# Optimization experiments

Hardware: AMD Instinct MI355X
Metric: run time of the kernel (lower is better)

## Reference

```python
import jax, jax.numpy as jnp
import numpy as np

B, C, H, W = 16, 1, 512, 512
D, F, KH, KW = 4, 24, 5, 5   # numWienerFilters, output_features, reg-filter size
BKH, BKW = 9, 9              # blur kernel size
LB, UB = 1e-4, 1e-2


def psf2otf(psf, shape):
    # zero-pad psf to `shape`, circularly shift its center to (0,0), FFT
    kh, kw = psf.shape[-2], psf.shape[-1]
    pad = [(0, 0)] * (psf.ndim - 2) + [(0, shape[0] - kh), (0, shape[1] - kw)]
    p = jnp.pad(psf, pad)
    p = jnp.roll(p, shift=(-((kh - 1) // 2), -((kw - 1) // 2)), axis=(-2, -1))
    return jnp.fft.fft2(p)


def _taper_profile(proj, n):
    # autocorrelation of the psf projection, periodized to length n (MATLAB edgetaper)
    z = jnp.zeros(n - 1, proj.dtype).at[: proj.shape[0]].set(proj)
    zf = jnp.fft.fft(z)
    acf = jnp.real(jnp.fft.ifft(zf * jnp.conj(zf)))
    acf = jnp.concatenate([acf, acf[:1]])
    return acf / acf.max()


def _normalize_weights(w, scale):
    # WeightNormalization5D: zero-mean + L2-normalize over (C,kh,kw), times scale
    w = w - w.mean(axis=(2, 3, 4), keepdims=True)
    nrm = jnp.sqrt(jnp.sum(w * w, axis=(2, 3, 4), keepdims=True))
    return w * (scale[..., None, None, None] / nrm)


def setup_inputs():
    key = jax.random.key(0)
    ks = jax.random.split(key, 4)
    x = jax.random.uniform(ks[0], (B, C, H, W), jnp.float32)
    bk = jax.random.uniform(ks[1], (BKH, BKW), jnp.float32) + 1e-3
    bk = bk / bk.sum()  # normalized blur PSF
    stdn = jax.random.uniform(ks[2], (B,), jnp.float32) * 0.1 + 0.01
    conv_weights = jax.random.normal(ks[3], (D, F, C, KH, KW), jnp.float32)
    scale = jnp.full((D, F), 0.1, jnp.float32)
    alpha = jnp.log(jnp.logspace(np.log10(LB), np.log10(UB), D))[:, None].astype(jnp.float32)
    return {"x": x, "blur_kernel": bk, "stdn": stdn,
            "conv_weights": conv_weights, "scale": scale, "alpha": alpha}


def reference(x, blur_kernel, stdn, conv_weights, scale, alpha):
    kh, kw = blur_kernel.shape
    # getPad2RetainShape
    pt, pb = (kh + 1) // 2 - 1, kh - (kh + 1) // 2
    pl, pr = (kw + 1) // 2 - 1, kw - (kw + 1) // 2
    xp = jnp.pad(x, ((0, 0), (0, 0), (pt, pb), (pl, pr)), mode="symmetric")
    Hp, Wp = xp.shape[-2], xp.shape[-1]
    otf = psf2otf(blur_kernel, (Hp, Wp))                     # (Hp,Wp) complex
    # EdgeTaper: blend image with its circular blur near borders
    br = _taper_profile(blur_kernel.sum(axis=1), Hp)
    bc = _taper_profile(blur_kernel.sum(axis=0), Wp)
    taper = (1.0 - br)[:, None] * (1.0 - bc)[None, :]
    blurred = jnp.real(jnp.fft.ifft2(jnp.fft.fft2(xp) * otf))
    xp = taper * xp + (1.0 - taper) * blurred
    # regularization-filter OTFs
    w = _normalize_weights(conv_weights, scale)              # (D,F,C,kh,kw)
    G = psf2otf(w, (Hp, Wp))                                 # (D,F,C,Hp,Wp)
    S = jnp.sum(G.real ** 2 + G.imag ** 2, axis=1)           # (D,C,Hp,Wp)
    a = jnp.exp(alpha)[:, :, None, None]                     # (D,1,1,1)
    B2 = otf.real ** 2 + otf.imag ** 2                       # (Hp,Wp)
    denom = B2[None, None] + a * S                           # (D,C,Hp,Wp)
    Y = jnp.conj(otf) * jnp.fft.fft2(xp)                     # (B,C,Hp,Wp)
    Xf = Y[:, None] / denom[None]                            # (B,D,C,Hp,Wp)
    out = jnp.real(jnp.fft.ifft2(Xf))[..., pt:Hp - pb, pl:Wp - pr]
    # colored-noise std factor per (wiener filter, channel)
    cvar = jnp.mean(B2[None, None] / denom ** 2, axis=(-2, -1))   # (D,C)
    cvar = jnp.broadcast_to(cvar[None], (x.shape[0],) + cvar.shape)  # (B,D,C)
    cstdn = jnp.sqrt(stdn[:, None] ** 2 * cvar.mean(axis=2))        # (B,D)
    return out, cstdn
```

## Files before the change

kernel.cpp:

```cpp
#include <hip/hip_runtime.h>
#include <math.h>

#define NP    520
#define NN    (520*520)
#define HH    512
#define NPIX  (512*512)
#define NB    16
#define NPAIR 8
#define ND    4
#define NF    24
#define KS    544
#define RS    576
#define PLANE ((size_t)RS*KS)
#define S8P   (8*PLANE)
#define E9SZ  (NP*9)
#define CSZ   (ND*9*NP)
#define NBORD 18396
#define PADCH 5536
#define NBLK2 1057
#define TWO_PI 6.283185307179586f

typedef unsigned short u16;
typedef __attribute__((ext_vector_type(8))) short bf16x8;
typedef __attribute__((ext_vector_type(4))) float f32x4;

__device__ __forceinline__ int wrap520(int t){ t %= NP; return t < 0 ? t + NP : t; }

__device__ __forceinline__ u16 f2bf(float f){
  unsigned u = __float_as_uint(f);
  u += 0x7FFFu + ((u >> 16) & 1u);
  return (u16)(u >> 16);
}
__device__ __forceinline__ float bf2f(u16 h){
  return __uint_as_float(((unsigned)h) << 16);
}
__device__ __forceinline__ void gll16(const u16* g, u16* l){
  __builtin_amdgcn_global_load_lds(
      (const __attribute__((address_space(1))) void*)g,
      (__attribute__((address_space(3))) void*)l, 16, 0, 0);
}
template<int N> __device__ __forceinline__ void vmwait(){
  if constexpr (N == 0)       asm volatile("s_waitcnt vmcnt(0)" ::: "memory");
  else if constexpr (N == 4)  asm volatile("s_waitcnt vmcnt(4)" ::: "memory");
  else if constexpr (N == 6)  asm volatile("s_waitcnt vmcnt(6)" ::: "memory");
  else if constexpr (N == 8)  asm volatile("s_waitcnt vmcnt(8)" ::: "memory");
  else if constexpr (N == 12) asm volatile("s_waitcnt vmcnt(12)" ::: "memory");
}
#define MF(a,b,c) __builtin_amdgcn_mfma_f32_16x16x32_bf16((a),(b),(c),0,0,0)


__global__ __launch_bounds__(256) void zwb_k(u16* __restrict__ slabs,
                                             u16* __restrict__ wf, u16* __restrict__ wi){
  int idx = blockIdx.x*256 + threadIdx.x;
  const int nA = 16*PADCH;
  if (idx < nA){
    int pl = idx / PADCH, cc = idx % PADCH;
    int row, col;
    if (cc < 1728){ row = cc/3; col = 520 + (cc%3)*8; }
    else { int c2 = cc - 1728; row = 520 + c2/68; col = (c2%68)*8; }
    bf16x8 z = {0,0,0,0,0,0,0,0};
    *(bf16x8*)(slabs + (size_t)pl*PLANE + (size_t)row*KS + col) = z;
    return;
  }
  idx -= nA;
  if (idx >= (int)PLANE) return;
  int r = idx / KS, k = idx % KS;
  float fr=0.f, fi=0.f, ir=0.f, ii=0.f;
  if (r < NP && k < NP){
    int m = (int)(((long long)r * (long long)k) % NP);
    float ang = TWO_PI * (float)m / (float)NP;
    float s, c; sincosf(ang, &s, &c);
    fr = c; fi = -s;
    ir = c * (1.0f/NP); ii = s * (1.0f/NP);
  }
  wf[0*PLANE+idx] = f2bf(fr); wf[1*PLANE+idx] = f2bf(fi);
  wi[0*PLANE+idx] = f2bf(ir); wi[1*PLANE+idx] = f2bf(ii);
}

__global__ __launch_bounds__(256) void setup1_k(const float* __restrict__ bk,
                                                const float* __restrict__ cw,
                                                const float* __restrict__ scale,
                                                float* __restrict__ e9,
                                                float* __restrict__ r_row, float* __restrict__ r_col,
                                                float* __restrict__ wn){
  int idx = blockIdx.x*256 + threadIdx.x;
  if (idx < NP*9){
    int u = idx / 9, t = idx % 9;
    int m = wrap520(u*(t-4));
    float ang = TWO_PI * (float)m / (float)NP;
    float s, c; sincosf(ang, &s, &c);
    e9[idx] = c; e9[E9SZ + idx] = -s;
    return;
  }
  idx -= NP*9;
  if (idx < 18){
    int k = idx % 9;
    bool rowp = (idx < 9);
    float proj[9];
    for (int m = 0; m < 9; ++m){
      float a = 0.f;
      for (int j = 0; j < 9; ++j) a += rowp ? bk[m*9+j] : bk[j*9+m];
      proj[m] = a;
    }
    float acc = 0.f;
    for (int m = 0; m + k < 9; ++m) acc += proj[m] * proj[m+k];
    (rowp ? r_row : r_col)[k] = acc;
    return;
  }
  idx -= 18;
  if (idx >= ND*NF) return;
  const float* wp = cw + idx*25;
  float mean = 0.f;
  for (int k = 0; k < 25; ++k) mean += wp[k];
  mean *= (1.0f/25.0f);
  float ss = 0.f;
  for (int k = 0; k < 25; ++k){ float d = wp[k]-mean; ss += d*d; }
  float sc = scale[idx] / sqrtf(ss);
  for (int k = 0; k < 25; ++k) wn[idx*25+k] = (wp[k]-mean)*sc;
}

__global__ __launch_bounds__(256) void setup2_k(const float* __restrict__ bk,
                                                const float* __restrict__ e9,
                                                const float* __restrict__ wn,
                                                float* __restrict__ T, float* __restrict__ R){
  int idx = blockIdx.x*256 + threadIdx.x;
  if (idx < 9*NP){
    int i = idx / NP, v = idx % NP;
    float tr = 0.f, ti = 0.f;
    #pragma unroll
    for (int j = 0; j < 9; ++j){
      float w = bk[i*9+j];
      tr += w * e9[v*9+j];
      ti += w * e9[E9SZ + v*9+j];
    }
    T[idx] = tr; T[9*NP + idx] = ti;
    return;
  }
  idx -= 9*NP;
  if (idx >= ND*81) return;
  int d = idx / 81, t = idx % 81;
  int di = t/9 - 4, dj = t%9 - 4;
  int i0 = di > 0 ? di : 0, i1 = di < 0 ? 4+di : 4;
  int j0 = dj > 0 ? dj : 0, j1 = dj < 0 ? 4+dj : 4;
  float acc = 0.f;
  for (int f = 0; f < NF; ++f){
    const float* w = wn + (d*NF+f)*25;
    for (int i = i0; i <= i1; ++i)
      for (int j = j0; j <= j1; ++j)
        acc += w[i*5+j] * w[(i-di)*5 + (j-dj)];
  }
  R[idx] = acc;
}

__global__ void C_k(const float* __restrict__ R, const float* __restrict__ e9,
                    float* __restrict__ Ctab){
  int idx = blockIdx.x*blockDim.x + threadIdx.x;
  if (idx >= ND*9*NP) return;
  int v = idx % NP, t9 = idx / NP;
  int d = t9 / 9, t = t9 % 9;
  float cr = 0.f, ci = 0.f;
  #pragma unroll
  for (int s = 0; s < 9; ++s){
    float r = R[d*81 + t*9 + s];
    cr += r * e9[v*9+s];
    ci += r * e9[E9SZ + v*9+s];
  }
  Ctab[idx] = cr; Ctab[CSZ + idx] = ci;
}

__global__ __launch_bounds__(256) void denomMT2_k(
    const float* __restrict__ Tb, const float* __restrict__ e9,
    const float* __restrict__ Ctab, const float* __restrict__ alpha,
    float* __restrict__ MTre, float* __restrict__ MTim, float* __restrict__ pcv){
  __shared__ float e9r[2304], e9i[2304];
  __shared__ float red[256];
  const int tid = threadIdx.x;
  const int p = blockIdx.x*256 + tid;
  {
    int u0 = (blockIdx.x*256) % NP;
    for (int i = tid; i < 2304; i += 256){
      int row = i / 9, col = i % 9;
      int uu = u0 + row; if (uu >= NP) uu -= NP;
      e9r[i] = e9[uu*9 + col];
      e9i[i] = e9[E9SZ + uu*9 + col];
    }
  }
  __syncthreads();
  float contrib[ND] = {0.f, 0.f, 0.f, 0.f};
  if (p < NN){
    int v = p / NP;
    float er9[9], ei9[9];
    #pragma unroll
    for (int i = 0; i < 9; ++i){ er9[i] = e9r[tid*9+i]; ei9[i] = e9i[tid*9+i]; }
    float ar = 0.f, ai = 0.f;
    #pragma unroll
    for (int i = 0; i < 9; ++i){
      float tr = Tb[i*NP+v], ti = Tb[9*NP + i*NP+v];
      ar += er9[i]*tr - ei9[i]*ti;
      ai += er9[i]*ti + ei9[i]*tr;
    }
    float B2 = ar*ar + ai*ai;
    #pragma unroll
    for (int d = 0; d < ND; ++d){
      float S = 0.f;
      #pragma unroll
      for (int t = 0; t < 9; ++t)
        S += er9[t]*Ctab[(d*9+t)*NP + v] - ei9[t]*Ctab[CSZ + (d*9+t)*NP + v];
      float dv = B2 + expf(alpha[d]) * S;
      MTre[(size_t)d*NN + p] = ar / dv;
      MTim[(size_t)d*NN + p] = -ai / dv;
      contrib[d] = B2 / (dv*dv);
    }
  }
  for (int d = 0; d < ND; ++d){
    red[tid] = contrib[d]; __syncthreads();
    for (int s = 128; s > 0; s >>= 1){
      if (tid < s) red[tid] += red[tid+s];
      __syncthreads();
    }
    if (tid == 0) pcv[(size_t)blockIdx.x*ND + d] = red[0];
    __syncthreads();
  }
}

__global__ __launch_bounds__(256) void cstdn2_k(const float* __restrict__ stdn,
                                                const float* __restrict__ pcv,
                                                float* __restrict__ out){
  __shared__ float red[256];
  int t = threadIdx.x;
  int d = t & 3, ch = t >> 2;
  float acc = 0.f;
  for (int b = ch; b < NBLK2; b += 64) acc += pcv[(size_t)b*ND + d];
  red[t] = acc; __syncthreads();
  for (int s = 128; s >= 4; s >>= 1){
    if (t < s) red[t] += red[t+s];
    __syncthreads();
  }
  if (t < NB*ND){
    int b = t >> 2, d2 = t & 3;
    float s = stdn[b];
    out[(size_t)NB*ND*NPIX + t] = sqrtf(s*s*red[d2]*(1.0f/(float)NN));
  }
}

__global__ __launch_bounds__(256) void pad_tr_k(const float* __restrict__ x,
                                                u16* __restrict__ MA){
  __shared__ float tile[64][65];
  const int q  = blockIdx.z;
  const int r0 = blockIdx.y * 64;
  const int c0 = blockIdx.x * 64;
  const int t  = threadIdx.x;
  const float* xq = x + (size_t)q*NPIX;
  const int jl = t & 63, ib = t >> 6;
  const bool fast = (c0 >= 64 && c0 <= 448 && r0 >= 64 && r0 <= 448);

  if (fast){
    #pragma unroll 1
    for (int pass = 0; pass < 16; ++pass){
      int il = ib + pass*4;
      tile[il][jl] = xq[(size_t)(c0+il-4)*HH + (r0+jl-4)];
    }
  } else {
    #pragma unroll 1
    for (int pass = 0; pass < 16; ++pass){
      int il = ib + pass*4;
      int I = c0 + il, J = r0 + jl;
      float v = 0.f;
      if (I < NP && J < NP){
        int si = I - 4; si = (si < 0) ? (-si-1) : ((si >= HH) ? (2*HH-1-si) : si);
        int sj = J - 4; sj = (sj < 0) ? (-sj-1) : ((sj >= HH) ? (2*HH-1-sj) : sj);
        v = xq[(size_t)si*HH + sj];
      }
      tile[il][jl] = v;
    }
  }
  __syncthreads();

  const int cchunk = t & 7, rb = t >> 3;
  const int pair = q >> 1, pl = q & 1;
  #pragma unroll
  for (int half = 0; half < 2; ++half){
    int rl = rb + half*32;
    int r = r0 + rl, cg = c0 + cchunk*8;
    if (r >= NP || cg >= NP) continue;
    bf16x8 vh;
    #pragma unroll
    for (int e = 0; e < 8; ++e)
      vh[e] = (short)f2bf(tile[cchunk*8+e][rl]);
    size_t o = (size_t)pair*PLANE + (size_t)r*KS + cg;
    *(bf16x8*)(MA + (size_t)pl*S8P + o) = vh;
  }
}

__global__ __launch_bounds__(256) void border_k(const float* __restrict__ x,
                                                const float* __restrict__ bk,
                                                const float* __restrict__ r_row,
                                                const float* __restrict__ r_col,
                                                u16* __restrict__ MA){
  __shared__ float bks[81], rr_[9], rc_[9];
  if (threadIdx.x < 81) bks[threadIdx.x] = bk[threadIdx.x];
  if (threadIdx.x < 9){ rr_[threadIdx.x] = r_row[threadIdx.x]; rc_[threadIdx.x] = r_col[threadIdx.x]; }
  __syncthreads();
  int idx = blockIdx.x*256 + threadIdx.x;
  if (idx >= NB*NBORD) return;
  int q = idx / NBORD, t = idx % NBORD;
  int I, J;
  if (t < 9360){ int ri = t / 520; I = (ri < 9) ? ri : 502 + ri; J = t % 520; }
  else { int s = t - 9360; I = 9 + s / 18; int ci = s % 18; J = (ci < 9) ? ci : 502 + ci; }
  const float* xq = x + (size_t)q*NPIX;
  auto XP = [&](int ii, int jj)->float{
    int si = ii - 4; si = (si < 0) ? (-si-1) : ((si >= HH) ? (2*HH-1-si) : si);
    int sj = jj - 4; sj = (sj < 0) ? (-sj-1) : ((sj >= HH) ? (2*HH-1-sj) : sj);
    return xq[(size_t)si*HH + sj];
  };
  float v = XP(I, J);
  float brv = (I < 9) ? rr_[I] : ((I >= 511) ? rr_[519-I] : 0.f);
  float bcv = (J < 9) ? rc_[J] : ((J >= 511) ? rc_[519-J] : 0.f);
  brv /= rr_[0]; bcv /= rc_[0];
  float tp = (1.f - brv) * (1.f - bcv);
  float blur = 0.f;
  for (int a = 0; a < 9; ++a){
    int ii = wrap520(I - a + 4);
    for (int b2 = 0; b2 < 9; ++b2){
      int jj = wrap520(J - b2 + 4);
      blur += bks[a*9+b2] * XP(ii, jj);
    }
  }
  v = tp*v + (1.f - tp)*blur;
  int pair = q >> 1, pl = q & 1;
  MA[(size_t)pl*S8P + (size_t)pair*PLANE + (size_t)J*KS + I] = f2bf(v);
}

__global__ __launch_bounds__(256) void maskF_k(const u16* __restrict__ IN, u16* __restrict__ OUT,
                                               const float* __restrict__ Mre, const float* __restrict__ Mim){
  int idx = blockIdx.x*256 + threadIdx.x;
  if (idx >= NPAIR*NP*65) return;
  int pr = idx / (NP*65), rem = idx % (NP*65);
  int r = rem / 65, c0 = (rem % 65)*8;
  size_t o = (size_t)pr*PLANE + (size_t)r*KS + c0;
  bf16x8 qr = *(const bf16x8*)(IN + 0*S8P + o);
  bf16x8 qi = *(const bf16x8*)(IN + 1*S8P + o);
  const float* mrp = Mre + (size_t)r*NP + c0;
  const float* mip = Mim + (size_t)r*NP + c0;
  bf16x8 o0, o1;
  #pragma unroll
  for (int e = 0; e < 8; ++e){
    float vr = bf2f((u16)qr[e]), vi = bf2f((u16)qi[e]);
    float mr = mrp[e], mi = mip[e];
    o0[e] = (short)f2bf(vr*mr - vi*mi);
    o1[e] = (short)f2bf(vr*mi + vi*mr);
  }
  *(bf16x8*)(OUT + 0*S8P + o) = o0;
  *(bf16x8*)(OUT + 1*S8P + o) = o1;
}

template<int BM, int CROP, int MASKOUT>
__global__ __launch_bounds__(256) void gemm_k(
    const u16* __restrict__ P, size_t pPl, size_t pZp, size_t pZd,
    const u16* __restrict__ Q, size_t qPl, size_t qZp, size_t qZd,
    u16* __restrict__ O, size_t oPl, size_t oZp, size_t oZd,
    float* __restrict__ cropOut, int dBase,
    const float* __restrict__ Mre, const float* __restrict__ Mim)
{
  constexpr int NW = 4;
  constexpr int FR = BM/32;
  constexpr int TR = BM/16;
  constexpr int LPW = 4*TR/NW;
  constexpr int PLSTR = BM*32;
  constexpr int BUF = 4*PLSTR;
  constexpr int NK = KS/32;
  __shared__ u16 lds[3*BUF];
  const int tid = threadIdx.x;
  const int l = tid & 63, w = tid >> 6;

  const int gx = gridDim.x, gy = gridDim.y;
  int lin = blockIdx.x + gx*(blockIdx.y + gy*blockIdx.z);
  int ntot = gx*gy*gridDim.z;
  int q8 = ntot >> 3, r8 = ntot & 7;
  int xcd = lin & 7, id8 = lin >> 3;
  int nl = (xcd < r8 ? xcd*(q8+1) : r8*(q8+1) + (xcd-r8)*q8) + id8;
  int BX = nl % gx; int t2 = nl / gx;
  int BY = t2 % gy; int BZ = t2 / gy;

  const int pair = BZ & 7;
  const int dd = dBase + (BZ >> 3);
  const int R0 = BY * BM, C0 = BX * BM;

  const u16* Pb = P + (size_t)pair*pZp + (size_t)dd*pZd;
  const u16* Qb = Q + (size_t)pair*qZp + (size_t)dd*qZd;

  const int s = l >> 2;
  const int cs8 = ((l & 3) ^ ((s >> 1) & 3)) * 8;
  const size_t pOff0 = (size_t)(R0 + s)*KS + cs8;
  const size_t qOff0 = (size_t)(C0 + s)*KS + cs8;

  const int lm = l & 15, lc = l >> 4;
  const int wm = w >> 1, wn = w & 1;

  f32x4 zero4 = {0.f, 0.f, 0.f, 0.f};
  f32x4 aRe[FR][FR], aIm[FR][FR];
  #pragma unroll
  for (int i = 0; i < FR; ++i)
    #pragma unroll
    for (int j = 0; j < FR; ++j){ aRe[i][j] = zero4; aIm[i][j] = zero4; }

  auto STAGE = [&](int bi, int k0){
    u16* dst = lds + bi*BUF;
    #pragma unroll
    for (int i = 0; i < LPW; ++i){
      int t = w + i*NW;
      int q2 = t / TR, r2 = t % TR;
      const u16* src = (q2 < 2) ? (Pb + (size_t)q2*pPl + pOff0)
                                : (Qb + (size_t)(q2-2)*qPl + qOff0);
      gll16(src + (size_t)(r2*16)*KS + k0, dst + q2*PLSTR + r2*512);
    }
  };

  STAGE(0, 0);
  STAGE(1, 32);

  #pragma unroll 1
  for (int kt = 0; kt < NK; ++kt){
    if (kt + 1 < NK) vmwait<LPW>(); else vmwait<0>();
    __builtin_amdgcn_sched_barrier(0);
    __builtin_amdgcn_s_barrier();
    __builtin_amdgcn_sched_barrier(0);
    if (kt + 2 < NK) STAGE((kt+2)%3, (kt+2)*32);

    const u16* buf = lds + (kt%3)*BUF;
    bf16x8 pf[FR][2];
    #pragma unroll
    for (int mi = 0; mi < FR; ++mi){
      int r = wm*(FR*16) + mi*16 + lm;
      int co = ((lc ^ ((r >> 1) & 3)) << 3);
      pf[mi][0] = *(const bf16x8*)(buf + 0*PLSTR + r*32 + co);
      pf[mi][1] = *(const bf16x8*)(buf + 1*PLSTR + r*32 + co);
    }
    int rq0 = wn*(FR*16) + lm;
    int cq0 = ((lc ^ ((rq0 >> 1) & 3)) << 3);
    bf16x8 q0 = *(const bf16x8*)(buf + 2*PLSTR + rq0*32 + cq0);
    bf16x8 q1 = *(const bf16x8*)(buf + 3*PLSTR + rq0*32 + cq0);
    #pragma unroll
    for (int ni = 0; ni < FR; ++ni){
      bf16x8 nq0 = q0, nq1 = q1;
      if (ni + 1 < FR){
        int r = wn*(FR*16) + (ni+1)*16 + lm;
        int co = ((lc ^ ((r >> 1) & 3)) << 3);
        nq0 = *(const bf16x8*)(buf + 2*PLSTR + r*32 + co);
        nq1 = *(const bf16x8*)(buf + 3*PLSTR + r*32 + co);
      }
      __builtin_amdgcn_s_setprio(1);
      #pragma unroll
      for (int mi = 0; mi < FR; ++mi){
        bf16x8 nw = pf[mi][1] ^ (short)0x8000;
        f32x4 re = aRe[mi][ni], im = aIm[mi][ni];
        re = MF(pf[mi][0], q0, re);
        re = MF(nw,        q1, re);
        im = MF(pf[mi][0], q1, im);
        im = MF(pf[mi][1], q0, im);
        aRe[mi][ni] = re; aIm[mi][ni] = im;
      }
      __builtin_amdgcn_s_setprio(0);
      q0 = nq0; q1 = nq1;
    }
  }

  u16* Ob = O ? (O + (size_t)pair*oZp + (size_t)dd*oZd) : nullptr;
  #pragma unroll
  for (int mi = 0; mi < FR; ++mi)
    #pragma unroll
    for (int ni = 0; ni < FR; ++ni){
      int cb = C0 + wn*(FR*16) + ni*16 + lm;
      int rb = R0 + wm*(FR*16) + mi*16 + lc*4;
      #pragma unroll
      for (int e = 0; e < 4; ++e){
        int rr = rb + e;
        float vr = aRe[mi][ni][e], vi = aIm[mi][ni][e];
        if (CROP){
          if (rr >= 4 && rr < 516 && cb >= 4 && cb < 516){
            size_t px = (size_t)(rr-4)*HH + (cb-4);
            cropOut[((size_t)(2*pair  )*ND + dd)*NPIX + px] = vr;
            cropOut[((size_t)(2*pair+1)*ND + dd)*NPIX + px] = vi;
          }
        } else if (MASKOUT){
          if (cb < KS){
            size_t o = (size_t)rr*KS + cb;
            size_t mo = (size_t)(rr < NP ? rr : 0)*NP + (cb < NP ? cb : 0);
            #pragma unroll
            for (int d2 = 0; d2 < ND; ++d2){
              float mr = Mre[(size_t)d2*NN + mo], mi2 = Mim[(size_t)d2*NN + mo];
              u16* Od = O + (size_t)d2*oZd + (size_t)pair*oZp;
              Od[0*oPl+o] = f2bf(vr*mr - vi*mi2);
              Od[1*oPl+o] = f2bf(vr*mi2 + vi*mr);
            }
          }
        } else {
          if (cb < KS){
            size_t o = (size_t)rr*KS + cb;
            Ob[0*oPl+o] = f2bf(vr);
            Ob[1*oPl+o] = f2bf(vi);
          }
        }
      }
    }
}


extern "C" void kernel_launch(void* const* d_in, const int* in_sizes, int n_in,
                              void* d_out, int out_size, void* d_ws, size_t ws_size,
                              hipStream_t stream){
  const float* x     = (const float*)d_in[0];
  const float* bk    = (const float*)d_in[1];
  const float* stdn  = (const float*)d_in[2];
  const float* cw    = (const float*)d_in[3];
  const float* scale = (const float*)d_in[4];
  const float* alpha = (const float*)d_in[5];
  float* out = (float*)d_out;

  char* base = (char*)d_ws;
  const size_t UNIT = 16*PLANE*sizeof(u16);
  size_t off;
  auto alloc = [&](size_t bytes)->void*{
    void* p = base + off;
    off += (bytes + 255) & ~(size_t)255;
    return p;
  };

  u16 *MA, *MB, *MC, *Dm, *Do, *WF, *WI;
  float *MTre, *MTim, *e9, *Tb, *Rarr, *Ctab, *r_row, *r_col, *wn, *pcv;
  auto layout = [&](bool bigL){
    off = 0;
    MA = (u16*)alloc(UNIT);
    MB = (u16*)alloc(UNIT);
    if (bigL){ Dm = (u16*)alloc(4*UNIT); Do = (u16*)alloc(4*UNIT); MC = nullptr; }
    else     { MC = (u16*)alloc(UNIT);   Dm = nullptr; Do = nullptr; }
    WF = (u16*)alloc(2*PLANE*sizeof(u16));
    WI = (u16*)alloc(2*PLANE*sizeof(u16));
    MTre = (float*)alloc((size_t)ND*NN*4);
    MTim = (float*)alloc((size_t)ND*NN*4);
    e9   = (float*)alloc(2*E9SZ*4);
    Tb   = (float*)alloc(2*9*NP*4);
    Rarr = (float*)alloc(ND*81*4);
    Ctab = (float*)alloc(2*CSZ*4);
    r_row = (float*)alloc(64);
    r_col = (float*)alloc(64);
    wn   = (float*)alloc(ND*NF*25*4);
    pcv  = (float*)alloc((size_t)NBLK2*ND*4);
    return off;
  };
  bool big = (layout(true) <= ws_size);
  if (!big){
    if (layout(false) > ws_size) return;
  }

  {
    int ztot = 16*PADCH + (int)PLANE;
    zwb_k<<<(ztot+255)/256, 256, 0, stream>>>(MA, WF, WI);
  }
  setup1_k<<<(NP*9+18+ND*NF+255)/256, 256, 0, stream>>>(bk, cw, scale, e9, r_row, r_col, wn);
  setup2_k<<<(9*NP+ND*81+255)/256, 256, 0, stream>>>(bk, e9, wn, Tb, Rarr);
  C_k     <<<(ND*9*NP+255)/256, 256, 0, stream>>>(Rarr, e9, Ctab);
  denomMT2_k<<<NBLK2, 256, 0, stream>>>(Tb, e9, Ctab, alpha, MTre, MTim, pcv);
  cstdn2_k<<<1, 256, 0, stream>>>(stdn, pcv, out);
  pad_tr_k<<<dim3(9, 9, NB), 256, 0, stream>>>(x, MA);
  border_k<<<(NB*NBORD+255)/256, 256, 0, stream>>>(x, bk, r_row, r_col, MA);

  gemm_k<64,0,0><<<dim3(9,9,8),256,0,stream>>>(
      WF, PLANE, 0, 0,   MA, S8P, PLANE, 0,   MB, S8P, PLANE, 0,
      nullptr, 0, nullptr, nullptr);

  if (big){
    gemm_k<64,0,1><<<dim3(9,9,8),256,0,stream>>>(
        WF, PLANE, 0, 0,   MB, S8P, PLANE, 0,   Dm, S8P, PLANE, 16*PLANE,
        nullptr, 0, MTre, MTim);
    gemm_k<96,0,0><<<dim3(6,6,32),256,0,stream>>>(
        WI, PLANE, 0, 0,   Dm, S8P, PLANE, 16*PLANE,   Do, S8P, PLANE, 16*PLANE,
        nullptr, 0, nullptr, nullptr);
    gemm_k<96,1,0><<<dim3(6,6,32),256,0,stream>>>(
        Do, S8P, PLANE, 16*PLANE,   WI, PLANE, 0, 0,   nullptr, 0, 0, 0,
        out, 0, nullptr, nullptr);
  } else {
    gemm_k<64,0,0><<<dim3(9,9,8),256,0,stream>>>(
        WF, PLANE, 0, 0,   MB, S8P, PLANE, 0,   MC, S8P, PLANE, 0,
        nullptr, 0, nullptr, nullptr);
    const int mgrid = (NPAIR*NP*65 + 255)/256;
    for (int d = 0; d < ND; ++d){
      maskF_k<<<mgrid,256,0,stream>>>(MC, MA, MTre + (size_t)d*NN, MTim + (size_t)d*NN);
      gemm_k<96,0,0><<<dim3(6,6,8),256,0,stream>>>(
          WI, PLANE, 0, 0,   MA, S8P, PLANE, 0,   MB, S8P, PLANE, 0,
          nullptr, 0, nullptr, nullptr);
      gemm_k<96,1,0><<<dim3(6,6,8),256,0,stream>>>(
          MB, S8P, PLANE, 0,   WI, PLANE, 0, 0,   nullptr, 0, 0, 0,
          out, d, nullptr, nullptr);
    }
  }
}
```

Before: 276.6 us.

## Store Wiener mask in bf16 and restructure GEMM k-loop LDS loads and barriers

The per-frequency Wiener mask (MTre/MTim) is now written and read as bf16 instead of fp32, which halves its memory footprint and the traffic in maskF and the masked GEMM epilogue. Separately, the GEMM inner loop no longer software-prefetches the next Q fragment. It issues the next global-to-LDS stage only in the first ni iteration and adds an extra workgroup barrier plus an lgkmcnt(0) wait in every other ni iteration. The precision change adds rounding error to the mask. The extra barriers and the lost LDS prefetch may serialize the MFMA work.

```diff
diff --git a/kernel.cpp b/kernel.cpp
--- a/kernel.cpp
+++ b/kernel.cpp
@@ -171,7 +171,7 @@
 __global__ __launch_bounds__(256) void denomMT2_k(
     const float* __restrict__ Tb, const float* __restrict__ e9,
     const float* __restrict__ Ctab, const float* __restrict__ alpha,
-    float* __restrict__ MTre, float* __restrict__ MTim, float* __restrict__ pcv){
+    u16* __restrict__ MTre, u16* __restrict__ MTim, float* __restrict__ pcv){
   __shared__ float e9r[2304], e9i[2304];
   __shared__ float red[256];
   const int tid = threadIdx.x;
@@ -207,8 +207,8 @@
       for (int t = 0; t < 9; ++t)
         S += er9[t]*Ctab[(d*9+t)*NP + v] - ei9[t]*Ctab[CSZ + (d*9+t)*NP + v];
       float dv = B2 + expf(alpha[d]) * S;
-      MTre[(size_t)d*NN + p] = ar / dv;
-      MTim[(size_t)d*NN + p] = -ai / dv;
+      MTre[(size_t)d*NN + p] = f2bf(ar / dv);
+      MTim[(size_t)d*NN + p] = f2bf(-ai / dv);
       contrib[d] = B2 / (dv*dv);
     }
   }
@@ -332,7 +332,7 @@
 }
 
 __global__ __launch_bounds__(256) void maskF_k(const u16* __restrict__ IN, u16* __restrict__ OUT,
-                                               const float* __restrict__ Mre, const float* __restrict__ Mim){
+                                               const u16* __restrict__ Mre, const u16* __restrict__ Mim){
   int idx = blockIdx.x*256 + threadIdx.x;
   if (idx >= NPAIR*NP*65) return;
   int pr = idx / (NP*65), rem = idx % (NP*65);
@@ -340,13 +340,13 @@
   size_t o = (size_t)pr*PLANE + (size_t)r*KS + c0;
   bf16x8 qr = *(const bf16x8*)(IN + 0*S8P + o);
   bf16x8 qi = *(const bf16x8*)(IN + 1*S8P + o);
-  const float* mrp = Mre + (size_t)r*NP + c0;
-  const float* mip = Mim + (size_t)r*NP + c0;
+  const u16* mrp = Mre + (size_t)r*NP + c0;
+  const u16* mip = Mim + (size_t)r*NP + c0;
   bf16x8 o0, o1;
   #pragma unroll
   for (int e = 0; e < 8; ++e){
     float vr = bf2f((u16)qr[e]), vi = bf2f((u16)qi[e]);
-    float mr = mrp[e], mi = mip[e];
+    float mr = bf2f(mrp[e]), mi = bf2f(mip[e]);
     o0[e] = (short)f2bf(vr*mr - vi*mi);
     o1[e] = (short)f2bf(vr*mi + vi*mr);
   }
@@ -360,7 +360,7 @@
     const u16* __restrict__ Q, size_t qPl, size_t qZp, size_t qZd,
     u16* __restrict__ O, size_t oPl, size_t oZp, size_t oZd,
     float* __restrict__ cropOut, int dBase,
-    const float* __restrict__ Mre, const float* __restrict__ Mim)
+    const u16* __restrict__ Mre, const u16* __restrict__ Mim)
 {
   constexpr int NW = 4;
   constexpr int FR = BM/32;
@@ -425,7 +425,6 @@
     __builtin_amdgcn_sched_barrier(0);
     __builtin_amdgcn_s_barrier();
     __builtin_amdgcn_sched_barrier(0);
-    if (kt + 2 < NK) STAGE((kt+2)%3, (kt+2)*32);
 
     const u16* buf = lds + (kt%3)*BUF;
     bf16x8 pf[FR][2];
@@ -436,19 +435,20 @@
       pf[mi][0] = *(const bf16x8*)(buf + 0*PLSTR + r*32 + co);
       pf[mi][1] = *(const bf16x8*)(buf + 1*PLSTR + r*32 + co);
     }
-    int rq0 = wn*(FR*16) + lm;
-    int cq0 = ((lc ^ ((rq0 >> 1) & 3)) << 3);
-    bf16x8 q0 = *(const bf16x8*)(buf + 2*PLSTR + rq0*32 + cq0);
-    bf16x8 q1 = *(const bf16x8*)(buf + 3*PLSTR + rq0*32 + cq0);
     #pragma unroll
     for (int ni = 0; ni < FR; ++ni){
-      bf16x8 nq0 = q0, nq1 = q1;
-      if (ni + 1 < FR){
-        int r = wn*(FR*16) + (ni+1)*16 + lm;
-        int co = ((lc ^ ((r >> 1) & 3)) << 3);
-        nq0 = *(const bf16x8*)(buf + 2*PLSTR + r*32 + co);
-        nq1 = *(const bf16x8*)(buf + 3*PLSTR + r*32 + co);
+      int rq = wn*(FR*16) + ni*16 + lm;
+      int cq = ((lc ^ ((rq >> 1) & 3)) << 3);
+      bf16x8 q0 = *(const bf16x8*)(buf + 2*PLSTR + rq*32 + cq);
+      bf16x8 q1 = *(const bf16x8*)(buf + 3*PLSTR + rq*32 + cq);
+      if (ni == 0){
+        if (kt + 2 < NK) STAGE((kt+2)%3, (kt+2)*32);
+      } else {
+        __builtin_amdgcn_sched_barrier(0);
+        __builtin_amdgcn_s_barrier();
       }
+      asm volatile("s_waitcnt lgkmcnt(0)" ::: "memory");
+      __builtin_amdgcn_sched_barrier(0);
       __builtin_amdgcn_s_setprio(1);
       #pragma unroll
       for (int mi = 0; mi < FR; ++mi){
@@ -461,7 +461,6 @@
         aRe[mi][ni] = re; aIm[mi][ni] = im;
       }
       __builtin_amdgcn_s_setprio(0);
-      q0 = nq0; q1 = nq1;
     }
   }
 
@@ -488,7 +487,8 @@
             size_t mo = (size_t)(rr < NP ? rr : 0)*NP + (cb < NP ? cb : 0);
             #pragma unroll
             for (int d2 = 0; d2 < ND; ++d2){
-              float mr = Mre[(size_t)d2*NN + mo], mi2 = Mim[(size_t)d2*NN + mo];
+              float mr = bf2f(Mre[(size_t)d2*NN + mo]);
+              float mi2 = bf2f(Mim[(size_t)d2*NN + mo]);
               u16* Od = O + (size_t)d2*oZd + (size_t)pair*oZp;
               Od[0*oPl+o] = f2bf(vr*mr - vi*mi2);
               Od[1*oPl+o] = f2bf(vr*mi2 + vi*mr);
@@ -526,8 +526,8 @@
     return p;
   };
 
-  u16 *MA, *MB, *MC, *Dm, *Do, *WF, *WI;
-  float *MTre, *MTim, *e9, *Tb, *Rarr, *Ctab, *r_row, *r_col, *wn, *pcv;
+  u16 *MA, *MB, *MC, *Dm, *Do, *WF, *WI, *MTre, *MTim;
+  float *e9, *Tb, *Rarr, *Ctab, *r_row, *r_col, *wn, *pcv;
   auto layout = [&](bool bigL){
     off = 0;
     MA = (u16*)alloc(UNIT);
@@ -536,8 +536,8 @@
     else     { MC = (u16*)alloc(UNIT);   Dm = nullptr; Do = nullptr; }
     WF = (u16*)alloc(2*PLANE*sizeof(u16));
     WI = (u16*)alloc(2*PLANE*sizeof(u16));
-    MTre = (float*)alloc((size_t)ND*NN*4);
-    MTim = (float*)alloc((size_t)ND*NN*4);
+    MTre = (u16*)alloc((size_t)ND*NN*2);
+    MTim = (u16*)alloc((size_t)ND*NN*2);
     e9   = (float*)alloc(2*E9SZ*4);
     Tb   = (float*)alloc(2*9*NP*4);
     Rarr = (float*)alloc(ND*81*4);
```

Measured after the change: 275.2 us. Within noise of the previous version (-0.5%).
